# Kernel optimization log

Measured on AMD Instinct MI355X. Metric: run time of the kernel, lower is better.

## Reference

```python
import jax, jax.numpy as jnp
import numpy as np

N_RES = 4096
N_PAIRS = 500000

def setup_inputs() -> dict:
    key = jax.random.key(0)
    k1, k2, k3 = jax.random.split(key, 3)
    ca_coords = jax.random.normal(k1, (N_RES, 3), dtype=jnp.float32) * 10.0
    K = jax.random.uniform(k2, (N_RES, N_RES), dtype=jnp.float32)
    pairs = jax.random.randint(k3, (N_PAIRS, 2), 0, N_RES, dtype=jnp.int64)
    return {"ca_coords": ca_coords, "K": K, "pairs": pairs}


def _reconstruct_backbone(ca):
    # vectorized version of reconstruct_backbone_atoms
    n = ca.shape[0]
    vec = ca[1:] - ca[:-1]                                  # (n-1,3)
    unit = vec / (jnp.linalg.norm(vec, axis=-1, keepdims=True) + 1e-8)
    # N atoms: n_coords[i] = ca[i] - 0.38*unit(ca[i]-ca[i-1]); n_coords[0] uses unit[0]
    n_coords = jnp.concatenate([ca[:1] - 0.38 * unit[:1], ca[1:] - 0.38 * unit], axis=0)
    # C atoms: c_coords[i] = ca[i] + 0.38*unit(ca[i+1]-ca[i]); c_coords[-1] uses unit[-1]
    c_coords = jnp.concatenate([ca[:-1] + 0.38 * unit, ca[-1:] + 0.38 * unit[-1:]], axis=0)
    # O atoms: perpendicular to (C-CA, N-CA) plane, last residue special-cased
    vec_n = n_coords[:-1] - ca[:-1]
    vec_c = c_coords[:-1] - ca[:-1]
    perp = jnp.cross(vec_c, vec_n)
    pnorm = jnp.linalg.norm(perp, axis=-1, keepdims=True)
    perp = jnp.where(pnorm > 1e-6, perp / jnp.maximum(pnorm, 1e-12), perp)
    o_body = c_coords[:-1] + 1.24 * perp
    o_last = c_coords[-1:] + jnp.array([[0.0, 1.24, 0.0]], dtype=ca.dtype)
    o_coords = jnp.concatenate([o_body, o_last], axis=0)
    return n_coords, c_coords, o_coords


def _pairwise_dist(x, y):
    # safe cdist: sqrt clamped so diagonal zeros stay differentiable
    sq = jnp.sum((x[:, None, :] - y[None, :, :]) ** 2, axis=-1)
    return jnp.sqrt(jnp.maximum(sq, 1e-12))


def reference(ca_coords, K, pairs):
    n = ca_coords.shape[0]

    # --- bond energy (weight=30): mean((|ca[i+1]-ca[i]| - 3.8)^2) ---
    d_bond = jnp.linalg.norm(ca_coords[1:] - ca_coords[:-1], axis=-1)
    e_bond = 30.0 * jnp.mean((d_bond - 3.8) ** 2)

    # --- clash energy (weight=50): mean(relu(3.2 - d_pair)^2) ---
    dv = ca_coords[pairs[:, 0]] - ca_coords[pairs[:, 1]]
    d_pair = jnp.sqrt(jnp.maximum(jnp.sum(dv ** 2, axis=-1), 1e-12))
    e_clash = 50.0 * jnp.mean(jax.nn.relu(3.2 - d_pair) ** 2)

    # --- contact energy (weight=5): mean((D - 8*(1-K))^2) over full NxN ---
    D = _pairwise_dist(ca_coords, ca_coords)
    target = 8.0 * (1.0 - K)
    e_contact = 5.0 * jnp.mean((D - target) ** 2)

    # --- hydrogen bond energy (weight=4) from reconstructed backbone ---
    n_coords, c_coords, o_coords = _reconstruct_backbone(ca_coords)
    ideal = 2.95
    hb = jnp.float32(0.0)
    # double loop i, j in [i+2, i+6) -> offsets 2..5, vectorized per offset
    for off in (2, 3, 4, 5):
        d = jnp.linalg.norm(o_coords[: n - off] - n_coords[off:], axis=-1)
        pen = jnp.exp(-(((d - ideal) / 0.3) ** 2))
        hb = hb - 0.5 * jnp.sum(jnp.where((d > 2.5) & (d < 3.5), pen, 0.0))
    e_hb = 4.0 * hb / (n * n)

    return e_bond + e_clash + e_contact + e_hb
```

## Files before the change

kernel.cpp:

```cpp
#include <hip/hip_runtime.h>
#include <math.h>

#define NRES   4096
#define GRID   768
#define TROWS  4
#define NTILES (NRES / TROWS)
#define HB_BLOCKS (NRES / 256)

__device__ __forceinline__ float wave_sum(float v) {
#pragma unroll
    for (int off = 32; off > 0; off >>= 1) v += __shfl_down(v, off, 64);
    return v;
}

__device__ __forceinline__ float fsqrt(float x) { return __builtin_amdgcn_sqrtf(x); }

__device__ __forceinline__ float c4(float4 kv, float4 cx, float4 cy, float4 cz,
                                    float xi, float yi, float zi, float s) {
    float dx, dy, dz, D, t;
    dx = xi - cx.x; dy = yi - cy.x; dz = zi - cz.x;
    D  = fsqrt(fmaf(dx, dx, fmaf(dy, dy, dz * dz)));
    t  = fmaf(8.f, kv.x, D - 8.f);
    s  = fmaf(t, t, s);

    dx = xi - cx.y; dy = yi - cy.y; dz = zi - cz.y;
    D  = fsqrt(fmaf(dx, dx, fmaf(dy, dy, dz * dz)));
    t  = fmaf(8.f, kv.y, D - 8.f);
    s  = fmaf(t, t, s);

    dx = xi - cx.z; dy = yi - cy.z; dz = zi - cz.z;
    D  = fsqrt(fmaf(dx, dx, fmaf(dy, dy, dz * dz)));
    t  = fmaf(8.f, kv.z, D - 8.f);
    s  = fmaf(t, t, s);

    dx = xi - cx.w; dy = yi - cy.w; dz = zi - cz.w;
    D  = fsqrt(fmaf(dx, dx, fmaf(dy, dy, dz * dz)));
    t  = fmaf(8.f, kv.w, D - 8.f);
    s  = fmaf(t, t, s);
    return s;
}

__global__ __launch_bounds__(256, 3) void energy_kernel(const float* __restrict__ ca,
                                                        const float* __restrict__ K,
                                                        const int* __restrict__ pairs,
                                                        float4* __restrict__ partial,
                                                        int npairs) {
    __shared__ float sx[NRES], sy[NRES], sz[NRES];
    __shared__ float red[4][4];
    const int tid = threadIdx.x;
    const int b   = blockIdx.x;

    for (int j = tid; j < NRES; j += 256) {
        sx[j] = ca[3 * j + 0];
        sy[j] = ca[3 * j + 1];
        sz[j] = ca[3 * j + 2];
    }
    __syncthreads();

    float contact = 0.f;
    for (int t = b; t < NTILES; t += GRID) {
        const int rbase = t * TROWS;
        float xi[TROWS], yi[TROWS], zi[TROWS];
#pragma unroll
        for (int r = 0; r < TROWS; ++r) {
            xi[r] = sx[rbase + r]; yi[r] = sy[rbase + r]; zi[r] = sz[rbase + r];
        }

        const float* Kt = K + (size_t)rbase * NRES;
        const int j0 = tid << 2;
        float4 va[TROWS], vb[TROWS];
#pragma unroll
        for (int r = 0; r < TROWS; ++r)
            va[r] = *(const float4*)(Kt + (size_t)r * NRES + j0);

#pragma unroll
        for (int c = 0; c < 4; ++c) {
            const int jc = j0 + (c << 10);
            float4* cur = (c & 1) ? vb : va;
            float4* nxt = (c & 1) ? va : vb;
            if (c < 3) {
                const int jn = j0 + ((c + 1) << 10);
#pragma unroll
                for (int r = 0; r < TROWS; ++r)
                    nxt[r] = *(const float4*)(Kt + (size_t)r * NRES + jn);
            }
            const float4 cx = *(const float4*)&sx[jc];
            const float4 cy = *(const float4*)&sy[jc];
            const float4 cz = *(const float4*)&sz[jc];
#pragma unroll
            for (int r = 0; r < TROWS; ++r)
                contact = c4(cur[r], cx, cy, cz, xi[r], yi[r], zi[r], contact);
        }
    }

    float clash = 0.f;
    for (int p = b * 256 + tid; p < npairs; p += GRID * 256) {
        int2 pr = ((const int2*)pairs)[p];
        float dx = sx[pr.x] - sx[pr.y];
        float dy = sy[pr.x] - sy[pr.y];
        float dz = sz[pr.x] - sz[pr.y];
        float d  = fsqrt(fmaxf(fmaf(dx, dx, fmaf(dy, dy, dz * dz)), 1e-12f));
        float r  = fmaxf(3.2f - d, 0.f);
        clash = fmaf(r, r, clash);
    }

    float bond = 0.f, hb = 0.f;
    if (b < HB_BLOCKS) {
        const int i = b * 256 + tid;
        const int n = NRES;

        if (i < n - 1) {
            float dx = sx[i+1]-sx[i], dy = sy[i+1]-sy[i], dz = sz[i+1]-sz[i];
            float d  = sqrtf(fmaf(dx, dx, fmaf(dy, dy, dz * dz)));
            float t  = d - 3.8f;
            bond = t * t;
        }

        if (i < n - 2) {
            float cax = sx[i], cay = sy[i], caz = sz[i];
            float vx = sx[i+1]-cax, vy = sy[i+1]-cay, vz = sz[i+1]-caz;
            float inv = 1.f / (sqrtf(vx*vx + vy*vy + vz*vz) + 1e-8f);
            float ux = vx*inv, uy = vy*inv, uz = vz*inv;

            float upx, upy, upz;
            if (i == 0) { upx = ux; upy = uy; upz = uz; }
            else {
                float wx = cax-sx[i-1], wy = cay-sy[i-1], wz = caz-sz[i-1];
                float inv2 = 1.f / (sqrtf(wx*wx + wy*wy + wz*wz) + 1e-8f);
                upx = wx*inv2; upy = wy*inv2; upz = wz*inv2;
            }

            float vcx = 0.38f*ux,  vcy = 0.38f*uy,  vcz = 0.38f*uz;
            float vnx = -0.38f*upx, vny = -0.38f*upy, vnz = -0.38f*upz;
            float px = vcy*vnz - vcz*vny;
            float py = vcz*vnx - vcx*vnz;
            float pz = vcx*vny - vcy*vnx;
            float pn = sqrtf(px*px + py*py + pz*pz);
            if (pn > 1e-6f) {
                float ipn = 1.f / fmaxf(pn, 1e-12f);
                px *= ipn; py *= ipn; pz *= ipn;
            }
            float ox = cax + vcx + 1.24f*px;
            float oy = cay + vcy + 1.24f*py;
            float oz = caz + vcz + 1.24f*pz;

#pragma unroll
            for (int off = 2; off <= 5; ++off) {
                int jj = i + off;
                if (jj < n) {
                    float cjx = sx[jj], cjy = sy[jj], cjz = sz[jj];
                    float qx = cjx-sx[jj-1], qy = cjy-sy[jj-1], qz = cjz-sz[jj-1];
                    float invq = 1.f / (sqrtf(qx*qx + qy*qy + qz*qz) + 1e-8f);
                    float njx = cjx - 0.38f*qx*invq;
                    float njy = cjy - 0.38f*qy*invq;
                    float njz = cjz - 0.38f*qz*invq;
                    float ddx = ox-njx, ddy = oy-njy, ddz = oz-njz;
                    float d = sqrtf(ddx*ddx + ddy*ddy + ddz*ddz);
                    if (d > 2.5f && d < 3.5f) {
                        float z = (d - 2.95f) * (1.0f / 0.3f);
                        hb -= 0.5f * expf(-z*z);
                    }
                }
            }
        }
    }

    float vbo = wave_sum(bond);
    float vcl = wave_sum(clash);
    float vco = wave_sum(contact);
    float vhb = wave_sum(hb);
    const int wave = tid >> 6;
    if ((tid & 63) == 0) {
        red[wave][0] = vbo; red[wave][1] = vcl; red[wave][2] = vco; red[wave][3] = vhb;
    }
    __syncthreads();
    if (tid == 0) {
        float4 o;
        o.x = red[0][0] + red[1][0] + red[2][0] + red[3][0];
        o.y = red[0][1] + red[1][1] + red[2][1] + red[3][1];
        o.z = red[0][2] + red[1][2] + red[2][2] + red[3][2];
        o.w = red[0][3] + red[1][3] + red[2][3] + red[3][3];
        partial[b] = o;
    }
}

__global__ __launch_bounds__(256) void finalize_kernel(const float4* __restrict__ partial,
                                                       float* __restrict__ out,
                                                       int n, int npairs) {
    __shared__ float red[4][4];
    const int tid = threadIdx.x;
    float vb = 0.f, vc = 0.f, vk = 0.f, vh = 0.f;
#pragma unroll
    for (int s = 0; s < GRID; s += 256) {
        float4 a = partial[tid + s];
        vb += a.x; vc += a.y; vk += a.z; vh += a.w;
    }
    vb = wave_sum(vb); vc = wave_sum(vc); vk = wave_sum(vk); vh = wave_sum(vh);
    const int wave = tid >> 6;
    if ((tid & 63) == 0) {
        red[wave][0] = vb; red[wave][1] = vc; red[wave][2] = vk; red[wave][3] = vh;
    }
    __syncthreads();
    if (tid == 0) {
        float bond    = red[0][0] + red[1][0] + red[2][0] + red[3][0];
        float clash   = red[0][1] + red[1][1] + red[2][1] + red[3][1];
        float contact = red[0][2] + red[1][2] + red[2][2] + red[3][2];
        float hb      = red[0][3] + red[1][3] + red[2][3] + red[3][3];
        float inv_nn  = 1.f / ((float)n * (float)n);
        out[0] = 30.f * bond / (float)(n - 1)
               + 50.f * clash / (float)npairs
               + 5.f  * contact * inv_nn
               + 4.f  * hb * inv_nn;
    }
}

extern "C" void kernel_launch(void* const* d_in, const int* in_sizes, int n_in,
                              void* d_out, int out_size, void* d_ws, size_t ws_size,
                              hipStream_t stream) {
    const float* ca    = (const float*)d_in[0];
    const float* K     = (const float*)d_in[1];
    const int*   pairs = (const int*)d_in[2];
    float* out = (float*)d_out;
    float4* partial = (float4*)d_ws;

    int n      = in_sizes[0] / 3;
    int npairs = in_sizes[2] / 2;

    energy_kernel<<<GRID, 256, 0, stream>>>(ca, K, pairs, partial, npairs);
    finalize_kernel<<<1, 256, 0, stream>>>(partial, out, n, npairs);
}
```

Measured before the change: 101.3 us.

## Rebalance contact rows per block, nontemporal K loads, prefetch pairs before staging

Replaces the strided 4-row tile loop with a fixed assignment of 6 rows to the first 256 blocks and 5 rows to the rest, so every block takes a single pass and all 4096 rows are covered. K and pair indices are now read with nontemporal loads. The pair indices are fetched before the coordinate staging so their latency overlaps with it. The clash loop is unrolled to a fixed three iterations. This hardcodes the grid, NRES and a pair count below three times the grid stride, and drops the generic loop.

```diff
diff --git a/kernel.cpp b/kernel.cpp
--- a/kernel.cpp
+++ b/kernel.cpp
@@ -1,11 +1,13 @@
 #include <hip/hip_runtime.h>
 #include <math.h>
 
-#define NRES   4096
-#define GRID   768
-#define TROWS  4
-#define NTILES (NRES / TROWS)
+#define NRES 4096
+#define GRID 768
 #define HB_BLOCKS (NRES / 256)
+#define PSTRIDE (GRID * 256)
+
+typedef float  f32x4 __attribute__((ext_vector_type(4)));
+typedef int    i32x2 __attribute__((ext_vector_type(2)));
 
 __device__ __forceinline__ float wave_sum(float v) {
 #pragma unroll
@@ -15,28 +17,55 @@
 
 __device__ __forceinline__ float fsqrt(float x) { return __builtin_amdgcn_sqrtf(x); }
 
-__device__ __forceinline__ float c4(float4 kv, float4 cx, float4 cy, float4 cz,
+__device__ __forceinline__ float c4(f32x4 kv, f32x4 cx, f32x4 cy, f32x4 cz,
                                     float xi, float yi, float zi, float s) {
     float dx, dy, dz, D, t;
-    dx = xi - cx.x; dy = yi - cy.x; dz = zi - cz.x;
-    D  = fsqrt(fmaf(dx, dx, fmaf(dy, dy, dz * dz)));
-    t  = fmaf(8.f, kv.x, D - 8.f);
-    s  = fmaf(t, t, s);
-
-    dx = xi - cx.y; dy = yi - cy.y; dz = zi - cz.y;
-    D  = fsqrt(fmaf(dx, dx, fmaf(dy, dy, dz * dz)));
-    t  = fmaf(8.f, kv.y, D - 8.f);
-    s  = fmaf(t, t, s);
-
-    dx = xi - cx.z; dy = yi - cy.z; dz = zi - cz.z;
-    D  = fsqrt(fmaf(dx, dx, fmaf(dy, dy, dz * dz)));
-    t  = fmaf(8.f, kv.z, D - 8.f);
-    s  = fmaf(t, t, s);
-
-    dx = xi - cx.w; dy = yi - cy.w; dz = zi - cz.w;
-    D  = fsqrt(fmaf(dx, dx, fmaf(dy, dy, dz * dz)));
-    t  = fmaf(8.f, kv.w, D - 8.f);
-    s  = fmaf(t, t, s);
+#pragma unroll
+    for (int e = 0; e < 4; ++e) {
+        dx = xi - cx[e]; dy = yi - cy[e]; dz = zi - cz[e];
+        D  = fsqrt(fmaf(dx, dx, fmaf(dy, dy, dz * dz)));
+        t  = fmaf(8.f, kv[e], D - 8.f);
+        s  = fmaf(t, t, s);
+    }
+    return s;
+}
+
+template <int R>
+__device__ __forceinline__ float contact_rows(const float* __restrict__ K, int row0,
+                                              const float* sx, const float* sy,
+                                              const float* sz, int tid) {
+    float xi[R], yi[R], zi[R];
+#pragma unroll
+    for (int r = 0; r < R; ++r) {
+        xi[r] = sx[row0 + r]; yi[r] = sy[row0 + r]; zi[r] = sz[row0 + r];
+    }
+    const float* Kt = K + (size_t)row0 * NRES;
+    const int j0 = tid << 2;
+    float s = 0.f;
+
+    f32x4 va[R], vb[R];
+#pragma unroll
+    for (int r = 0; r < R; ++r)
+        va[r] = __builtin_nontemporal_load((const f32x4*)(Kt + (size_t)r * NRES + j0));
+
+#pragma unroll
+    for (int c = 0; c < 4; ++c) {
+        const int jc = j0 + (c << 10);
+        f32x4* cur = (c & 1) ? vb : va;
+        f32x4* nxt = (c & 1) ? va : vb;
+        if (c < 3) {
+            const int jn = j0 + ((c + 1) << 10);
+#pragma unroll
+            for (int r = 0; r < R; ++r)
+                nxt[r] = __builtin_nontemporal_load((const f32x4*)(Kt + (size_t)r * NRES + jn));
+        }
+        const f32x4 cx = *(const f32x4*)&sx[jc];
+        const f32x4 cy = *(const f32x4*)&sy[jc];
+        const f32x4 cz = *(const f32x4*)&sz[jc];
+#pragma unroll
+        for (int r = 0; r < R; ++r)
+            s = c4(cur[r], cx, cy, cz, xi[r], yi[r], zi[r], s);
+    }
     return s;
 }
 
@@ -50,6 +79,14 @@
     const int tid = threadIdx.x;
     const int b   = blockIdx.x;
 
+    const int pbase = b * 256 + tid;
+    const i32x2* pairs2 = (const i32x2*)pairs;
+    i32x2 pr0 = __builtin_nontemporal_load(&pairs2[pbase]);
+    i32x2 pr1 = __builtin_nontemporal_load(&pairs2[pbase + PSTRIDE]);
+    const bool has2 = (pbase + 2 * PSTRIDE) < npairs;
+    i32x2 pr2 = has2 ? __builtin_nontemporal_load(&pairs2[pbase + 2 * PSTRIDE])
+                     : (i32x2){0, 0};
+
     for (int j = tid; j < NRES; j += 256) {
         sx[j] = ca[3 * j + 0];
         sy[j] = ca[3 * j + 1];
@@ -57,51 +94,26 @@
     }
     __syncthreads();
 
-    float contact = 0.f;
-    for (int t = b; t < NTILES; t += GRID) {
-        const int rbase = t * TROWS;
-        float xi[TROWS], yi[TROWS], zi[TROWS];
-#pragma unroll
-        for (int r = 0; r < TROWS; ++r) {
-            xi[r] = sx[rbase + r]; yi[r] = sy[rbase + r]; zi[r] = sz[rbase + r];
-        }
-
-        const float* Kt = K + (size_t)rbase * NRES;
-        const int j0 = tid << 2;
-        float4 va[TROWS], vb[TROWS];
-#pragma unroll
-        for (int r = 0; r < TROWS; ++r)
-            va[r] = *(const float4*)(Kt + (size_t)r * NRES + j0);
-
-#pragma unroll
-        for (int c = 0; c < 4; ++c) {
-            const int jc = j0 + (c << 10);
-            float4* cur = (c & 1) ? vb : va;
-            float4* nxt = (c & 1) ? va : vb;
-            if (c < 3) {
-                const int jn = j0 + ((c + 1) << 10);
-#pragma unroll
-                for (int r = 0; r < TROWS; ++r)
-                    nxt[r] = *(const float4*)(Kt + (size_t)r * NRES + jn);
-            }
-            const float4 cx = *(const float4*)&sx[jc];
-            const float4 cy = *(const float4*)&sy[jc];
-            const float4 cz = *(const float4*)&sz[jc];
-#pragma unroll
-            for (int r = 0; r < TROWS; ++r)
-                contact = c4(cur[r], cx, cy, cz, xi[r], yi[r], zi[r], contact);
-        }
-    }
+    float contact;
+    if (b < 256) contact = contact_rows<6>(K, b * 6, sx, sy, sz, tid);
+    else         contact = contact_rows<5>(K, 1536 + (b - 256) * 5, sx, sy, sz, tid);
 
     float clash = 0.f;
-    for (int p = b * 256 + tid; p < npairs; p += GRID * 256) {
-        int2 pr = ((const int2*)pairs)[p];
-        float dx = sx[pr.x] - sx[pr.y];
-        float dy = sy[pr.x] - sy[pr.y];
-        float dz = sz[pr.x] - sz[pr.y];
-        float d  = fsqrt(fmaxf(fmaf(dx, dx, fmaf(dy, dy, dz * dz)), 1e-12f));
-        float r  = fmaxf(3.2f - d, 0.f);
-        clash = fmaf(r, r, clash);
+    {
+        float dx, dy, dz, d, r;
+        dx = sx[pr0.x] - sx[pr0.y]; dy = sy[pr0.x] - sy[pr0.y]; dz = sz[pr0.x] - sz[pr0.y];
+        d = fsqrt(fmaxf(fmaf(dx, dx, fmaf(dy, dy, dz * dz)), 1e-12f));
+        r = fmaxf(3.2f - d, 0.f); clash = fmaf(r, r, clash);
+
+        dx = sx[pr1.x] - sx[pr1.y]; dy = sy[pr1.x] - sy[pr1.y]; dz = sz[pr1.x] - sz[pr1.y];
+        d = fsqrt(fmaxf(fmaf(dx, dx, fmaf(dy, dy, dz * dz)), 1e-12f));
+        r = fmaxf(3.2f - d, 0.f); clash = fmaf(r, r, clash);
+
+        if (has2) {
+            dx = sx[pr2.x] - sx[pr2.y]; dy = sy[pr2.x] - sy[pr2.y]; dz = sz[pr2.x] - sz[pr2.y];
+            d = fsqrt(fmaxf(fmaf(dx, dx, fmaf(dy, dy, dz * dz)), 1e-12f));
+            r = fmaxf(3.2f - d, 0.f); clash = fmaf(r, r, clash);
+        }
     }
 
     float bond = 0.f, hb = 0.f;
```

After: 106.8 us. 1.05x slower.
